# Performance work log

Measured on AMD Instinct MI355X. Metric: run time of the kernel, lower is better.

## Reference

```python
import jax, jax.numpy as jnp
import numpy as np

N_NODES = 100000
N_EDGES = 800000
IN_DIM, HID_DIM, OUT_DIM = 128, 64, 7


def setup_inputs() -> dict:
    key = jax.random.key(0)
    ks = jax.random.split(key, 8)
    x = jax.random.normal(ks[0], (N_NODES, IN_DIM), dtype=jnp.float32)
    edge_index = jax.random.randint(ks[1], (2, N_EDGES), 0, N_NODES, dtype=jnp.int64)
    # Glorot-ish init for weights, zeros for bias (PyG GCNConv default)
    def glorot(k, shape):
        lim = float(np.sqrt(6.0 / (shape[0] + shape[1])))
        return jax.random.uniform(k, shape, dtype=jnp.float32, minval=-lim, maxval=lim)
    return {
        "x": x,
        "edge_index": edge_index,
        "W1": glorot(ks[2], (IN_DIM, HID_DIM)),
        "b1": jnp.zeros((HID_DIM,), jnp.float32),
        "W2": glorot(ks[3], (HID_DIM, HID_DIM)),
        "b2": jnp.zeros((HID_DIM,), jnp.float32),
        "W3": glorot(ks[4], (HID_DIM, OUT_DIM)),
        "b3": jnp.zeros((OUT_DIM,), jnp.float32),
    }


def _gcn_conv(h_in, src, dst, W, b, n_nodes):
    # PyG GCNConv: h = x @ W; add self-loops; D^-1/2 A_hat D^-1/2 aggregation; + b
    h = h_in @ W  # [N, F_out]
    # degree over destination nodes, +1 for self-loop
    deg = jax.ops.segment_sum(jnp.ones_like(dst, dtype=h.dtype), dst,
                              num_segments=n_nodes) + 1.0
    dinv = jax.lax.rsqrt(deg)  # [N]
    coef = dinv[src] * dinv[dst]  # [E]
    msg = h[src] * coef[:, None]  # gather + scale  [E, F_out]
    out = jax.ops.segment_sum(msg, dst, num_segments=n_nodes)  # scatter-add
    out = out + h * (dinv * dinv)[:, None]  # self-loop contribution
    return out + b


def reference(x, edge_index, W1, b1, W2, b2, W3, b3):
    src, dst = edge_index[0], edge_index[1]
    n = x.shape[0]
    h = jax.nn.relu(_gcn_conv(x, src, dst, W1, b1, n))
    # dropout(p=0.5) is identity in eval mode
    h = jax.nn.relu(_gcn_conv(h, src, dst, W2, b2, n))
    return _gcn_conv(h, src, dst, W3, b3, n)
```

## Files before the change

### kernel.cpp

```cpp
#include <hip/hip_runtime.h>

#define N_NODES 100000
#define N_EDGES 800000
#define IN_DIM 128
#define HID 64
#define OUT_DIM 7
#define CAP 32
#define NGROUP 8
#define DSLICE (N_NODES / NGROUP)
#define SUBBLK 390
#define NB_N ((N_NODES + 255) / 256)

typedef __bf16 vbf8 __attribute__((ext_vector_type(8)));
typedef float  vf4  __attribute__((ext_vector_type(4)));

__device__ __forceinline__ void wswz_body(int idx, const float* __restrict__ W,
                                          __bf16* __restrict__ out) {
    int j  = idx & 7;
    int l  = (idx >> 3) & 63;
    int nt = (idx >> 9) & 3;
    int ks = idx >> 11;
    int k  = ks * 32 + ((l >> 4) << 3) + j;
    int n  = nt * 16 + (l & 15);
    out[idx] = (__bf16)W[k * 64 + n];
}

__global__ __launch_bounds__(256)
void k_init(int* __restrict__ cnt, const float* __restrict__ W1,
            __bf16* __restrict__ Wz1, const float* __restrict__ W2,
            __bf16* __restrict__ Wz2) {
    int b = blockIdx.x;
    if (b < NB_N) {
        int i = b * 256 + threadIdx.x;
        if (i < N_NODES) cnt[i] = 0;
    } else if (b < NB_N + 32) {
        wswz_body((b - NB_N) * 256 + threadIdx.x, W1, Wz1);
    } else {
        wswz_body((b - NB_N - 32) * 256 + threadIdx.x, W2, Wz2);
    }
}

template<int K, bool F32IN>
__device__ __forceinline__ void gemm_mfma_body(int g, int tid,
                                               const void* __restrict__ Xv,
                                               const __bf16* __restrict__ Wswz,
                                               __bf16* __restrict__ Hb) {
    constexpr int KS = K / 32;
    const int lane = tid & 63;
    const int w = g * 4 + (tid >> 6);
    if (w >= N_NODES / 16) return;
    const int r0 = w * 16;
    const int m = lane & 15;
    const int quad = lane >> 4;

    vbf8 bfrag[KS][4];
    const vbf8* wp = (const vbf8*)Wswz;
    #pragma unroll
    for (int ks = 0; ks < KS; ++ks)
        #pragma unroll
        for (int nt = 0; nt < 4; ++nt)
            bfrag[ks][nt] = wp[(ks * 4 + nt) * 64 + lane];

    vf4 acc[4] = {};
    #pragma unroll
    for (int ks = 0; ks < KS; ++ks) {
        vbf8 a;
        if (F32IN) {
            const float* xp = (const float*)Xv + (size_t)(r0 + m) * K + ks * 32 + quad * 8;
            float4 f0 = *(const float4*)xp;
            float4 f1 = *(const float4*)(xp + 4);
            a[0] = (__bf16)f0.x; a[1] = (__bf16)f0.y; a[2] = (__bf16)f0.z; a[3] = (__bf16)f0.w;
            a[4] = (__bf16)f1.x; a[5] = (__bf16)f1.y; a[6] = (__bf16)f1.z; a[7] = (__bf16)f1.w;
        } else {
            a = *(const vbf8*)((const __bf16*)Xv + (size_t)(r0 + m) * K + ks * 32 + quad * 8);
        }
        #pragma unroll
        for (int nt = 0; nt < 4; ++nt)
            acc[nt] = __builtin_amdgcn_mfma_f32_16x16x32_bf16(a, bfrag[ks][nt], acc[nt], 0, 0, 0);
    }
    #pragma unroll
    for (int nt = 0; nt < 4; ++nt)
        #pragma unroll
        for (int r = 0; r < 4; ++r)
            Hb[(size_t)(r0 + quad * 4 + r) * 64 + nt * 16 + m] = (__bf16)acc[nt][r];
}

#define FILL_BLKS (NGROUP * SUBBLK)
#define GEMM_BLKS ((N_NODES / 16 + 3) / 4)
__global__ __launch_bounds__(256)
void k_build_gemm1(const int* __restrict__ ei, int* __restrict__ cnt,
                   int* __restrict__ csr, const float* __restrict__ X,
                   const __bf16* __restrict__ Wz1, __bf16* __restrict__ Hb) {
    int b = blockIdx.x;
    if (b < FILL_BLKS) {
        int group = b & 7, sub = b >> 3;
        int lo = group * DSLICE;
        const int4* dst4 = (const int4*)(ei + N_EDGES);
        for (int e4 = sub * 256 + threadIdx.x; e4 < N_EDGES / 4; e4 += SUBBLK * 256) {
            int4 d4 = dst4[e4];
            bool m0 = (unsigned)(d4.x - lo) < (unsigned)DSLICE;
            bool m1 = (unsigned)(d4.y - lo) < (unsigned)DSLICE;
            bool m2 = (unsigned)(d4.z - lo) < (unsigned)DSLICE;
            bool m3 = (unsigned)(d4.w - lo) < (unsigned)DSLICE;
            if (!(m0 | m1 | m2 | m3)) continue;
            int e = e4 * 4;
            if (m0) { int s = ei[e];     int p = atomicAdd(&cnt[d4.x], 1); if (p < CAP) csr[(size_t)d4.x * CAP + p] = s; }
            if (m1) { int s = ei[e + 1]; int p = atomicAdd(&cnt[d4.y], 1); if (p < CAP) csr[(size_t)d4.y * CAP + p] = s; }
            if (m2) { int s = ei[e + 2]; int p = atomicAdd(&cnt[d4.z], 1); if (p < CAP) csr[(size_t)d4.z * CAP + p] = s; }
            if (m3) { int s = ei[e + 3]; int p = atomicAdd(&cnt[d4.w], 1); if (p < CAP) csr[(size_t)d4.w * CAP + p] = s; }
        }
    } else {
        gemm_mfma_body<IN_DIM, true>(b - FILL_BLKS, threadIdx.x, X, Wz1, Hb);
    }
}

__global__ __launch_bounds__(256)
void k_gemm2(const __bf16* __restrict__ Ab, const __bf16* __restrict__ Wz2,
             __bf16* __restrict__ Hb) {
    gemm_mfma_body<HID, false>(blockIdx.x, threadIdx.x, Ab, Wz2, Hb);
}

__global__ __launch_bounds__(256)
void k_gather64(const int* __restrict__ cnt, const int* __restrict__ csr,
                const float* __restrict__ bias, const __bf16* __restrict__ Hb,
                __bf16* __restrict__ Ab) {
    int node = blockIdx.x * 32 + (threadIdx.x >> 3);
    int q = threadIdx.x & 7;
    if (node >= N_NODES) return;
    int deg = cnt[node];
    int end = deg < CAP ? deg : CAP;
    float dd = rsqrtf((float)deg + 1.0f);
    float d2 = dd * dd;
    vbf8 h8 = *(const vbf8*)(Hb + (size_t)node * 64 + q * 8);
    float4 b0 = *(const float4*)(bias + q * 8);
    float4 b1 = *(const float4*)(bias + q * 8 + 4);
    float acc[8];
    acc[0] = fmaf((float)h8[0], d2, b0.x); acc[1] = fmaf((float)h8[1], d2, b0.y);
    acc[2] = fmaf((float)h8[2], d2, b0.z); acc[3] = fmaf((float)h8[3], d2, b0.w);
    acc[4] = fmaf((float)h8[4], d2, b1.x); acc[5] = fmaf((float)h8[5], d2, b1.y);
    acc[6] = fmaf((float)h8[6], d2, b1.z); acc[7] = fmaf((float)h8[7], d2, b1.w);

    const int4* row4 = (const int4*)(csr + (size_t)node * CAP);
    int4 qa = row4[0], qb = row4[1], qc = row4[2], qd = row4[3];
    int srcs[16] = {qa.x, qa.y, qa.z, qa.w, qb.x, qb.y, qb.z, qb.w,
                    qc.x, qc.y, qc.z, qc.w, qd.x, qd.y, qd.z, qd.w};
    #pragma unroll
    for (int t = 0; t < 16; ++t) {
        bool live = t < end;
        int s = live ? srcs[t] : node;
        int cs = cnt[s];
        vbf8 v = *(const vbf8*)(Hb + (size_t)s * 64 + q * 8);
        float c = live ? rsqrtf((float)cs + 1.0f) * dd : 0.0f;
        #pragma unroll
        for (int u = 0; u < 8; ++u) acc[u] = fmaf((float)v[u], c, acc[u]);
    }
    for (int j = 16; j < end; ++j) {
        int s = (csr + (size_t)node * CAP)[j];
        float c = rsqrtf((float)cnt[s] + 1.0f) * dd;
        vbf8 v = *(const vbf8*)(Hb + (size_t)s * 64 + q * 8);
        #pragma unroll
        for (int u = 0; u < 8; ++u) acc[u] = fmaf((float)v[u], c, acc[u]);
    }
    vbf8 o;
    #pragma unroll
    for (int t = 0; t < 8; ++t) o[t] = (__bf16)fmaxf(acc[t], 0.f);
    *(vbf8*)(Ab + (size_t)node * 64 + q * 8) = o;
}

__global__ __launch_bounds__(256)
void k_gemm3(const __bf16* __restrict__ Ab, const float* __restrict__ W,
             const float* __restrict__ bias, const int* __restrict__ cnt,
             float* __restrict__ S, float* __restrict__ Out) {
    int row = blockIdx.x * blockDim.x + threadIdx.x;
    if (row >= N_NODES) return;
    float c[7] = {};
    const vbf8* xr = (const vbf8*)(Ab + (size_t)row * 64);
    #pragma unroll
    for (int k0 = 0; k0 < 8; ++k0) {
        vbf8 a = xr[k0];
        #pragma unroll
        for (int t = 0; t < 8; ++t) {
            float av = (float)a[t];
            #pragma unroll
            for (int j = 0; j < 7; ++j)
                c[j] = fmaf(av, W[(size_t)(k0 * 8 + t) * 7 + j], c[j]);
        }
    }
    float dd = rsqrtf((float)cnt[row] + 1.0f);
    float d2 = dd * dd;
    #pragma unroll
    for (int j = 0; j < 7; ++j) {
        S[(size_t)row * 7 + j] = c[j];
        Out[(size_t)row * 7 + j] = fmaf(c[j], d2, bias[j]);
    }
}

__global__ __launch_bounds__(256)
void k_gather7(const int* __restrict__ cnt, const int* __restrict__ csr,
               const float* __restrict__ S, float* __restrict__ Out) {
    int node = blockIdx.x * 32 + (threadIdx.x >> 3);
    int j7 = threadIdx.x & 7;
    if (node >= N_NODES || j7 >= 7) return;
    int deg = cnt[node];
    int end = deg < CAP ? deg : CAP;
    float dd = rsqrtf((float)deg + 1.0f);
    const int4* row4 = (const int4*)(csr + (size_t)node * CAP);
    int4 qa = row4[0], qb = row4[1], qc = row4[2], qd = row4[3];
    int srcs[16] = {qa.x, qa.y, qa.z, qa.w, qb.x, qb.y, qb.z, qb.w,
                    qc.x, qc.y, qc.z, qc.w, qd.x, qd.y, qd.z, qd.w};
    float acc = Out[(size_t)node * 7 + j7];
    #pragma unroll
    for (int t = 0; t < 16; ++t) {
        bool live = t < end;
        int s = live ? srcs[t] : node;
        int cs = cnt[s];
        float v = S[(size_t)s * 7 + j7];
        float c = live ? rsqrtf((float)cs + 1.0f) * dd : 0.0f;
        acc = fmaf(v, c, acc);
    }
    for (int j = 16; j < end; ++j) {
        int s = (csr + (size_t)node * CAP)[j];
        float c = rsqrtf((float)cnt[s] + 1.0f) * dd;
        acc = fmaf(S[(size_t)s * 7 + j7], c, acc);
    }
    Out[(size_t)node * 7 + j7] = acc;
}

static inline size_t align256(size_t x) { return (x + 255) & ~(size_t)255; }

extern "C" void kernel_launch(void* const* d_in, const int* in_sizes, int n_in,
                              void* d_out, int out_size, void* d_ws, size_t ws_size,
                              hipStream_t stream) {
    const float* x  = (const float*)d_in[0];
    const int*   ei = (const int*)d_in[1];
    const float* W1 = (const float*)d_in[2];
    const float* b1 = (const float*)d_in[3];
    const float* W2 = (const float*)d_in[4];
    const float* b2 = (const float*)d_in[5];
    const float* W3 = (const float*)d_in[6];
    const float* b3 = (const float*)d_in[7];
    float* out = (float*)d_out;

    char* wsp = (char*)d_ws;
    int*    cnt  = (int*)wsp;    wsp += align256(sizeof(int) * N_NODES);
    int*    csr  = (int*)wsp;    wsp += align256(sizeof(int) * (size_t)N_NODES * CAP);
    __bf16* Wz1  = (__bf16*)wsp; wsp += align256(sizeof(__bf16) * IN_DIM * 64);
    __bf16* Wz2  = (__bf16*)wsp; wsp += align256(sizeof(__bf16) * HID * 64);
    __bf16* HbA  = (__bf16*)wsp; wsp += align256(sizeof(__bf16) * (size_t)N_NODES * 64);
    __bf16* Ab   = (__bf16*)wsp; wsp += align256(sizeof(__bf16) * (size_t)N_NODES * 64);
    __bf16* HbB  = (__bf16*)wsp; wsp += align256(sizeof(__bf16) * (size_t)N_NODES * 64);
    float*  bufS = (float*)wsp;  wsp += align256(sizeof(float) * (size_t)N_NODES * 7);

    k_init<<<NB_N + 48, 256, 0, stream>>>(cnt, W1, Wz1, W2, Wz2);
    k_build_gemm1<<<FILL_BLKS + GEMM_BLKS, 256, 0, stream>>>(ei, cnt, csr, x, Wz1, HbA);
    k_gather64<<<N_NODES / 32, 256, 0, stream>>>(cnt, csr, b1, HbA, Ab);
    k_gemm2<<<GEMM_BLKS, 256, 0, stream>>>(Ab, Wz2, HbB);
    k_gather64<<<N_NODES / 32, 256, 0, stream>>>(cnt, csr, b2, HbB, Ab);
    k_gemm3<<<NB_N, 256, 0, stream>>>(Ab, W3, b3, cnt, bufS, out);
    k_gather7<<<N_NODES / 32, 256, 0, stream>>>(cnt, csr, bufS, out);
}
```

Measured before the change: 232.8 us.

## Build CSR in per-block LDS slices instead of global atomics

Each build block now owns a 640-node destination slice. It scans the full edge list and bins incoming edges with LDS atomics into a 16-entry local CSR, then copies counts and rows to global memory with vectorised stores. Slots past 16, up to the cap of 32, are written directly to global memory. Because counts are now written by the build blocks, the zeroing pass in the init kernel is removed. The aim is to avoid contended global atomics and scattered global writes, but every one of roughly 157 blocks rereads the whole destination array, which greatly increases cache traffic and makes each block's loop long and latency-bound.

```diff
diff --git a/kernel.cpp b/kernel.cpp
--- a/kernel.cpp
+++ b/kernel.cpp
@@ -6,9 +6,9 @@
 #define HID 64
 #define OUT_DIM 7
 #define CAP 32
-#define NGROUP 8
-#define DSLICE (N_NODES / NGROUP)
-#define SUBBLK 390
+#define CAP_LDS 16
+#define SL_NODES 640
+#define SL_BLOCKS ((N_NODES + SL_NODES - 1) / SL_NODES)
 #define NB_N ((N_NODES + 255) / 256)
 
 typedef __bf16 vbf8 __attribute__((ext_vector_type(8)));
@@ -26,18 +26,11 @@
 }
 
 __global__ __launch_bounds__(256)
-void k_init(int* __restrict__ cnt, const float* __restrict__ W1,
-            __bf16* __restrict__ Wz1, const float* __restrict__ W2,
-            __bf16* __restrict__ Wz2) {
+void k_init(const float* __restrict__ W1, __bf16* __restrict__ Wz1,
+            const float* __restrict__ W2, __bf16* __restrict__ Wz2) {
     int b = blockIdx.x;
-    if (b < NB_N) {
-        int i = b * 256 + threadIdx.x;
-        if (i < N_NODES) cnt[i] = 0;
-    } else if (b < NB_N + 32) {
-        wswz_body((b - NB_N) * 256 + threadIdx.x, W1, Wz1);
-    } else {
-        wswz_body((b - NB_N - 32) * 256 + threadIdx.x, W2, Wz2);
-    }
+    if (b < 32) wswz_body(b * 256 + threadIdx.x, W1, Wz1);
+    else        wswz_body((b - 32) * 256 + threadIdx.x, W2, Wz2);
 }
 
 template<int K, bool F32IN>
@@ -85,32 +78,63 @@
             Hb[(size_t)(r0 + quad * 4 + r) * 64 + nt * 16 + m] = (__bf16)acc[nt][r];
 }
 
-#define FILL_BLKS (NGROUP * SUBBLK)
 #define GEMM_BLKS ((N_NODES / 16 + 3) / 4)
 __global__ __launch_bounds__(256)
 void k_build_gemm1(const int* __restrict__ ei, int* __restrict__ cnt,
                    int* __restrict__ csr, const float* __restrict__ X,
                    const __bf16* __restrict__ Wz1, __bf16* __restrict__ Hb) {
+    __shared__ int lcnt[SL_NODES];
+    __shared__ int lcsr[SL_NODES * CAP_LDS];
     int b = blockIdx.x;
-    if (b < FILL_BLKS) {
-        int group = b & 7, sub = b >> 3;
-        int lo = group * DSLICE;
+    if (b < SL_BLOCKS) {
+        const int lo = b * SL_NODES;
+        const int sz = (lo + SL_NODES <= N_NODES) ? SL_NODES : (N_NODES - lo);
+        for (int i = threadIdx.x; i < SL_NODES; i += 256) lcnt[i] = 0;
+        __syncthreads();
         const int4* dst4 = (const int4*)(ei + N_EDGES);
-        for (int e4 = sub * 256 + threadIdx.x; e4 < N_EDGES / 4; e4 += SUBBLK * 256) {
+        for (int e4 = threadIdx.x; e4 < N_EDGES / 4; e4 += 256) {
             int4 d4 = dst4[e4];
-            bool m0 = (unsigned)(d4.x - lo) < (unsigned)DSLICE;
-            bool m1 = (unsigned)(d4.y - lo) < (unsigned)DSLICE;
-            bool m2 = (unsigned)(d4.z - lo) < (unsigned)DSLICE;
-            bool m3 = (unsigned)(d4.w - lo) < (unsigned)DSLICE;
-            if (!(m0 | m1 | m2 | m3)) continue;
             int e = e4 * 4;
-            if (m0) { int s = ei[e];     int p = atomicAdd(&cnt[d4.x], 1); if (p < CAP) csr[(size_t)d4.x * CAP + p] = s; }
-            if (m1) { int s = ei[e + 1]; int p = atomicAdd(&cnt[d4.y], 1); if (p < CAP) csr[(size_t)d4.y * CAP + p] = s; }
-            if (m2) { int s = ei[e + 2]; int p = atomicAdd(&cnt[d4.z], 1); if (p < CAP) csr[(size_t)d4.z * CAP + p] = s; }
-            if (m3) { int s = ei[e + 3]; int p = atomicAdd(&cnt[d4.w], 1); if (p < CAP) csr[(size_t)d4.w * CAP + p] = s; }
+            int r;
+            r = d4.x - lo;
+            if ((unsigned)r < (unsigned)sz) {
+                int s = ei[e];
+                int p = atomicAdd(&lcnt[r], 1);
+                if (p < CAP_LDS) lcsr[r * CAP_LDS + p] = s;
+                else if (p < CAP) csr[(size_t)d4.x * CAP + p] = s;
+            }
+            r = d4.y - lo;
+            if ((unsigned)r < (unsigned)sz) {
+                int s = ei[e + 1];
+                int p = atomicAdd(&lcnt[r], 1);
+                if (p < CAP_LDS) lcsr[r * CAP_LDS + p] = s;
+                else if (p < CAP) csr[(size_t)d4.y * CAP + p] = s;
+            }
+            r = d4.z - lo;
+            if ((unsigned)r < (unsigned)sz) {
+                int s = ei[e + 2];
+                int p = atomicAdd(&lcnt[r], 1);
+                if (p < CAP_LDS) lcsr[r * CAP_LDS + p] = s;
+                else if (p < CAP) csr[(size_t)d4.z * CAP + p] = s;
+            }
+            r = d4.w - lo;
+            if ((unsigned)r < (unsigned)sz) {
+                int s = ei[e + 3];
+                int p = atomicAdd(&lcnt[r], 1);
+                if (p < CAP_LDS) lcsr[r * CAP_LDS + p] = s;
+                else if (p < CAP) csr[(size_t)d4.w * CAP + p] = s;
+            }
+        }
+        __syncthreads();
+        for (int i = threadIdx.x; i < sz; i += 256) cnt[lo + i] = lcnt[i];
+        const int4* l4 = (const int4*)lcsr;
+        int4* g4 = (int4*)csr;
+        for (int i = threadIdx.x; i < sz * 4; i += 256) {
+            int rr = i >> 2, qd = i & 3;
+            g4[(size_t)(lo + rr) * 8 + qd] = l4[i];
         }
     } else {
-        gemm_mfma_body<IN_DIM, true>(b - FILL_BLKS, threadIdx.x, X, Wz1, Hb);
+        gemm_mfma_body<IN_DIM, true>(b - SL_BLOCKS, threadIdx.x, X, Wz1, Hb);
     }
 }
 
@@ -251,8 +275,8 @@
     __bf16* HbB  = (__bf16*)wsp; wsp += align256(sizeof(__bf16) * (size_t)N_NODES * 64);
     float*  bufS = (float*)wsp;  wsp += align256(sizeof(float) * (size_t)N_NODES * 7);
 
-    k_init<<<NB_N + 48, 256, 0, stream>>>(cnt, W1, Wz1, W2, Wz2);
-    k_build_gemm1<<<FILL_BLKS + GEMM_BLKS, 256, 0, stream>>>(ei, cnt, csr, x, Wz1, HbA);
+    k_init<<<48, 256, 0, stream>>>(W1, Wz1, W2, Wz2);
+    k_build_gemm1<<<SL_BLOCKS + GEMM_BLKS, 256, 0, stream>>>(ei, cnt, csr, x, Wz1, HbA);
     k_gather64<<<N_NODES / 32, 256, 0, stream>>>(cnt, csr, b1, HbA, Ab);
     k_gemm2<<<GEMM_BLKS, 256, 0, stream>>>(Ab, Wz2, HbB);
     k_gather64<<<N_NODES / 32, 256, 0, stream>>>(cnt, csr, b2, HbB, Ab);
```

New measurement: 562.2 us. 2.41x slower.

## Fuse layer-3 GEMM into gather by aggregating first, and reorder fused build blocks

Applied to the files above, without the earlier changes.

The final layer now aggregates the 64-wide hidden features over neighbors and then applies the 64x7 weight, with a shuffle reduction across 8 lanes. This replaces the separate gemm3 kernel, the intermediate S buffer and the gather7 kernel. Each edge now gathers 128 bytes of bf16 per node instead of 28 bytes of fp32, so gather traffic rises while one launch and one round trip of S are removed. The fused build/gemm1 kernel also puts the GEMM blocks first in the grid.

```diff
diff --git a/kernel.cpp b/kernel.cpp
--- a/kernel.cpp
+++ b/kernel.cpp
@@ -92,8 +92,11 @@
                    int* __restrict__ csr, const float* __restrict__ X,
                    const __bf16* __restrict__ Wz1, __bf16* __restrict__ Hb) {
     int b = blockIdx.x;
-    if (b < FILL_BLKS) {
-        int group = b & 7, sub = b >> 3;
+    if (b < GEMM_BLKS) {
+        gemm_mfma_body<IN_DIM, true>(b, threadIdx.x, X, Wz1, Hb);
+    } else {
+        int bb = b - GEMM_BLKS;
+        int group = bb & 7, sub = bb >> 3;
         int lo = group * DSLICE;
         const int4* dst4 = (const int4*)(ei + N_EDGES);
         for (int e4 = sub * 256 + threadIdx.x; e4 < N_EDGES / 4; e4 += SUBBLK * 256) {
@@ -109,8 +112,6 @@
             if (m2) { int s = ei[e + 2]; int p = atomicAdd(&cnt[d4.z], 1); if (p < CAP) csr[(size_t)d4.z * CAP + p] = s; }
             if (m3) { int s = ei[e + 3]; int p = atomicAdd(&cnt[d4.w], 1); if (p < CAP) csr[(size_t)d4.w * CAP + p] = s; }
         }
-    } else {
-        gemm_mfma_body<IN_DIM, true>(b - FILL_BLKS, threadIdx.x, X, Wz1, Hb);
     }
 }
 
@@ -168,62 +169,61 @@
 }
 
 __global__ __launch_bounds__(256)
-void k_gemm3(const __bf16* __restrict__ Ab, const float* __restrict__ W,
-             const float* __restrict__ bias, const int* __restrict__ cnt,
-             float* __restrict__ S, float* __restrict__ Out) {
-    int row = blockIdx.x * blockDim.x + threadIdx.x;
-    if (row >= N_NODES) return;
-    float c[7] = {};
-    const vbf8* xr = (const vbf8*)(Ab + (size_t)row * 64);
-    #pragma unroll
-    for (int k0 = 0; k0 < 8; ++k0) {
-        vbf8 a = xr[k0];
-        #pragma unroll
-        for (int t = 0; t < 8; ++t) {
-            float av = (float)a[t];
-            #pragma unroll
-            for (int j = 0; j < 7; ++j)
-                c[j] = fmaf(av, W[(size_t)(k0 * 8 + t) * 7 + j], c[j]);
-        }
-    }
-    float dd = rsqrtf((float)cnt[row] + 1.0f);
-    float d2 = dd * dd;
-    #pragma unroll
-    for (int j = 0; j < 7; ++j) {
-        S[(size_t)row * 7 + j] = c[j];
-        Out[(size_t)row * 7 + j] = fmaf(c[j], d2, bias[j]);
-    }
-}
-
-__global__ __launch_bounds__(256)
-void k_gather7(const int* __restrict__ cnt, const int* __restrict__ csr,
-               const float* __restrict__ S, float* __restrict__ Out) {
+void k_gather_out(const int* __restrict__ cnt, const int* __restrict__ csr,
+                  const __bf16* __restrict__ Ab, const float* __restrict__ W3,
+                  const float* __restrict__ b3, float* __restrict__ Out) {
     int node = blockIdx.x * 32 + (threadIdx.x >> 3);
-    int j7 = threadIdx.x & 7;
-    if (node >= N_NODES || j7 >= 7) return;
+    int q = threadIdx.x & 7;
+    if (node >= N_NODES) return;
     int deg = cnt[node];
     int end = deg < CAP ? deg : CAP;
     float dd = rsqrtf((float)deg + 1.0f);
+    float d2 = dd * dd;
+    vbf8 h8 = *(const vbf8*)(Ab + (size_t)node * 64 + q * 8);
+    float acc[8];
+    #pragma unroll
+    for (int t = 0; t < 8; ++t) acc[t] = (float)h8[t] * d2;
+
     const int4* row4 = (const int4*)(csr + (size_t)node * CAP);
     int4 qa = row4[0], qb = row4[1], qc = row4[2], qd = row4[3];
     int srcs[16] = {qa.x, qa.y, qa.z, qa.w, qb.x, qb.y, qb.z, qb.w,
                     qc.x, qc.y, qc.z, qc.w, qd.x, qd.y, qd.z, qd.w};
-    float acc = Out[(size_t)node * 7 + j7];
     #pragma unroll
     for (int t = 0; t < 16; ++t) {
         bool live = t < end;
         int s = live ? srcs[t] : node;
         int cs = cnt[s];
-        float v = S[(size_t)s * 7 + j7];
+        vbf8 v = *(const vbf8*)(Ab + (size_t)s * 64 + q * 8);
         float c = live ? rsqrtf((float)cs + 1.0f) * dd : 0.0f;
-        acc = fmaf(v, c, acc);
+        #pragma unroll
+        for (int u = 0; u < 8; ++u) acc[u] = fmaf((float)v[u], c, acc[u]);
     }
     for (int j = 16; j < end; ++j) {
         int s = (csr + (size_t)node * CAP)[j];
         float c = rsqrtf((float)cnt[s] + 1.0f) * dd;
-        acc = fmaf(S[(size_t)s * 7 + j7], c, acc);
-    }
-    Out[(size_t)node * 7 + j7] = acc;
+        vbf8 v = *(const vbf8*)(Ab + (size_t)s * 64 + q * 8);
+        #pragma unroll
+        for (int u = 0; u < 8; ++u) acc[u] = fmaf((float)v[u], c, acc[u]);
+    }
+
+    float p[7] = {};
+    #pragma unroll
+    for (int t = 0; t < 8; ++t) {
+        #pragma unroll
+        for (int j = 0; j < 7; ++j)
+            p[j] = fmaf(acc[t], W3[(q * 8 + t) * 7 + j], p[j]);
+    }
+    #pragma unroll
+    for (int msk = 1; msk < 8; msk <<= 1)
+        #pragma unroll
+        for (int j = 0; j < 7; ++j)
+            p[j] += __shfl_xor(p[j], msk, 8);
+    if (q < 7) {
+        float v = p[0];
+        if (q == 1) v = p[1]; else if (q == 2) v = p[2]; else if (q == 3) v = p[3];
+        else if (q == 4) v = p[4]; else if (q == 5) v = p[5]; else if (q == 6) v = p[6];
+        Out[(size_t)node * 7 + q] = v + b3[q];
+    }
 }
 
 static inline size_t align256(size_t x) { return (x + 255) & ~(size_t)255; }
@@ -249,13 +249,11 @@
     __bf16* HbA  = (__bf16*)wsp; wsp += align256(sizeof(__bf16) * (size_t)N_NODES * 64);
     __bf16* Ab   = (__bf16*)wsp; wsp += align256(sizeof(__bf16) * (size_t)N_NODES * 64);
     __bf16* HbB  = (__bf16*)wsp; wsp += align256(sizeof(__bf16) * (size_t)N_NODES * 64);
-    float*  bufS = (float*)wsp;  wsp += align256(sizeof(float) * (size_t)N_NODES * 7);
 
     k_init<<<NB_N + 48, 256, 0, stream>>>(cnt, W1, Wz1, W2, Wz2);
-    k_build_gemm1<<<FILL_BLKS + GEMM_BLKS, 256, 0, stream>>>(ei, cnt, csr, x, Wz1, HbA);
+    k_build_gemm1<<<GEMM_BLKS + FILL_BLKS, 256, 0, stream>>>(ei, cnt, csr, x, Wz1, HbA);
     k_gather64<<<N_NODES / 32, 256, 0, stream>>>(cnt, csr, b1, HbA, Ab);
     k_gemm2<<<GEMM_BLKS, 256, 0, stream>>>(Ab, Wz2, HbB);
     k_gather64<<<N_NODES / 32, 256, 0, stream>>>(cnt, csr, b2, HbB, Ab);
-    k_gemm3<<<NB_N, 256, 0, stream>>>(Ab, W3, b3, cnt, bufS, out);
-    k_gather7<<<N_NODES / 32, 256, 0, stream>>>(cnt, csr, bufS, out);
-}
+    k_gather_out<<<N_NODES / 32, 256, 0, stream>>>(cnt, csr, Ab, W3, b3, out);
+}
```

Result: slower. 241.6 us (+3.7%).
